# Kernel tuning notes

Measured on AMD Instinct MI355X. Metric: run time of the kernel, lower is better.

## Reference

```python
import jax, jax.numpy as jnp
import numpy as np

CHUNK = 2048  # i-tile size; each block kernel slab is CHUNK x M (128 MB fp32), never the full N x M


def setup_inputs() -> dict:
    key = jax.random.key(0)
    k1, k2, k3, k4 = jax.random.split(key, 4)
    ls = jax.random.uniform(k1, (1,), dtype=jnp.float32)          # scalar lengthscale g (Pm(0,1))
    x = jax.random.normal(k2, (16384, 32), dtype=jnp.float32)     # Vi points
    y = jax.random.normal(k3, (16384, 32), dtype=jnp.float32)     # Vj points
    b = jax.random.normal(k4, (16384, 16), dtype=jnp.float32)     # Vj RHS
    return {"ls": ls, "x": x, "y": y, "b": b}


def reference(ls, x, y, b):
    # out[i] = sum_j exp(-g * ||x_i - y_j||^2) * b[j]   (KeOps Genred Sum over axis=1)
    g = ls[0]
    N, D = x.shape
    yn = jnp.sum(y * y, axis=1)  # [M]

    def blk(xc):  # xc: [CHUNK, D]
        xn = jnp.sum(xc * xc, axis=1, keepdims=True)                   # [CHUNK, 1]
        sq = jnp.maximum(xn + yn[None, :] - 2.0 * (xc @ y.T), 0.0)     # [CHUNK, M]
        return jnp.exp(-g * sq) @ b                                    # [CHUNK, Dv]

    out = jax.lax.map(blk, x.reshape(N // CHUNK, CHUNK, D))
    return out.reshape(N, b.shape[1])
```

## Files before the change

### kernel.cpp

```cpp
#include <hip/hip_runtime.h>


#define NPTS 16384
#define D    32
#define DV   16
#define IBLK 256
#define JSPLIT 16
#define JBLK 64
#define NTILE  (NPTS / JBLK)
#define TILES  (NTILE / JSPLIT)
#define REC    12800
#define YH_OFF 256
#define YL_OFF 5376
#define BT_OFF 10496
#define PTS    72
#define PART_F4 (NPTS * DV / 4)

typedef _Float16 half8   __attribute__((ext_vector_type(8)));
typedef __fp16   cvt2_t  __attribute__((ext_vector_type(2)));
typedef float    float4_t __attribute__((ext_vector_type(4)));
typedef unsigned int u32;
typedef unsigned int u32x2 __attribute__((ext_vector_type(2)));

__device__ __forceinline__ void async16(const void* g, void* l) {
  __builtin_amdgcn_global_load_lds((const __attribute__((address_space(1))) u32*)g,
                                   (__attribute__((address_space(3))) u32*)l, 16, 0, 0);
}

__device__ __forceinline__ void stage_tile(const char* __restrict__ g,
                                           char* __restrict__ l, int tid) {
  async16(g + tid * 16,         l + tid * 16);
  async16(g + 4096 + tid * 16,  l + 4096 + tid * 16);
  async16(g + 8192 + tid * 16,  l + 8192 + tid * 16);
  if (tid < 32) async16(g + 12288 + tid * 16, l + 12288 + tid * 16);
}

__device__ __forceinline__ void permswap32(u32& a, u32& b) {
#if __has_builtin(__builtin_amdgcn_permlane32_swap)
  u32x2 r = __builtin_amdgcn_permlane32_swap(a, b, false, false);
  a = r[0]; b = r[1];
#else
  asm("v_permlane32_swap_b32 %0, %1" : "+v"(a), "+v"(b));
#endif
}

__device__ __forceinline__ void permswap16(u32& a, u32& b) {
#if __has_builtin(__builtin_amdgcn_permlane16_swap)
  u32x2 r = __builtin_amdgcn_permlane16_swap(a, b, false, false);
  a = r[0]; b = r[1];
#else
  asm("v_permlane16_swap_b32 %0, %1" : "+v"(a), "+v"(b));
#endif
}

__global__ __launch_bounds__(256) void rbf_prologue(
    const float* __restrict__ ls, const float* __restrict__ y,
    const float* __restrict__ b, char* __restrict__ rec0,
    float* __restrict__ outz, int zero_out) {
  __shared__ _Float16 sbt[256][17];
  const int tid = threadIdx.x;
  const int j = blockIdx.x * 256 + tid;
  const int tt = j >> 6, jloc = j & 63;
  char* rec = rec0 + (size_t)tt * REC;
  const float nl2g = -ls[0] * 1.4426950408889634f;

  const float4* yp = (const float4*)(y + (size_t)j * D);
  float s = 0.f;
  _Float16 hi[32], lo[32];
  #pragma unroll
  for (int c = 0; c < 8; ++c) {
    float4 v = yp[c];
    float f[4] = {v.x, v.y, v.z, v.w};
    #pragma unroll
    for (int k = 0; k < 4; ++k) {
      s = fmaf(f[k], f[k], s);
      _Float16 h = (_Float16)f[k];
      hi[c*4+k] = h;
      lo[c*4+k] = (_Float16)(f[k] - (float)h);
    }
  }
  ((float*)rec)[jloc] = nl2g * s;
  #pragma unroll
  for (int c = 0; c < 4; ++c) {
    *(half8*)(rec + YH_OFF + jloc * 80 + c * 16) = *(half8*)&hi[c*8];
    *(half8*)(rec + YL_OFF + jloc * 80 + c * 16) = *(half8*)&lo[c*8];
  }

  const float4* bp = (const float4*)(b + (size_t)j * DV);
  #pragma unroll
  for (int c = 0; c < 4; ++c) {
    float4 v = bp[c];
    sbt[tid][c*4+0] = (_Float16)v.x; sbt[tid][c*4+1] = (_Float16)v.y;
    sbt[tid][c*4+2] = (_Float16)v.z; sbt[tid][c*4+3] = (_Float16)v.w;
  }
  __syncthreads();
  #pragma unroll
  for (int r = 0; r < 2; ++r) {
    int cch = r * 256 + tid;
    int t4 = cch >> 7, rem = cch & 127, v = rem >> 3, jg = rem & 7;
    _Float16 tmp[8];
    #pragma unroll
    for (int k = 0; k < 8; ++k) tmp[k] = sbt[t4*64 + jg*8 + k][v];
    *(half8*)(rec0 + (size_t)(blockIdx.x*4 + t4)*REC + BT_OFF + v*144 + jg*16) =
        *(half8*)tmp;
  }

  if (zero_out) {
    float4 z = {0.f, 0.f, 0.f, 0.f};
    float4* ozp = (float4*)outz;
    #pragma unroll
    for (int r = 0; r < 4; ++r) ozp[blockIdx.x * 1024 + r * 256 + tid] = z;
  }
}

template <int MODE>
__global__ __launch_bounds__(256) void rbf_mfma(
    const float* __restrict__ ls, const float* __restrict__ x,
    const char* __restrict__ rec0, float* __restrict__ out,
    float* __restrict__ part) {
  __shared__ __align__(16) char SB[2][REC];

  const int tid  = threadIdx.x;
  const int lane = tid & 63, w = tid >> 6;
  const int t = lane & 15, q = lane >> 4;
  const int iblk = blockIdx.x & 63, jseg = blockIdx.x >> 6;
  const int tseg = jseg * TILES;

  const float nl2g = -ls[0] * 1.4426950408889634f;
  const float m2g  = -2.0f * nl2g;

  half8 xh[4], xl[4];
  float xns[4];
  #pragma unroll
  for (int f = 0; f < 4; ++f) {
    const int row = iblk * IBLK + f * 64 + w * 16 + t;
    const float4* xp = (const float4*)(x + (size_t)row * D + q * 8);
    float4 a0 = xp[0], a1 = xp[1];
    float fv[8] = {a0.x,a0.y,a0.z,a0.w,a1.x,a1.y,a1.z,a1.w};
    float s = 0.f;
    #pragma unroll
    for (int k = 0; k < 8; ++k) {
      s = fmaf(fv[k], fv[k], s);
      float vv = m2g * fv[k];
      _Float16 h = (_Float16)vv;
      xh[f][k] = h;
      xl[f][k] = (_Float16)(vv - (float)h);
    }
    s += __shfl_xor(s, 16);
    s += __shfl_xor(s, 32);
    xns[f] = fmaf(nl2g, s, 14.0f);
  }

  float4_t acc[4] = {{0,0,0,0},{0,0,0,0},{0,0,0,0},{0,0,0,0}};

  stage_tile(rec0 + (size_t)tseg * REC, &SB[0][0], tid);
  __syncthreads();

  for (int k = 0; k < TILES; ++k) {
    if (k + 1 < TILES)
      stage_tile(rec0 + (size_t)(tseg + k + 1) * REC, &SB[(k + 1) & 1][0], tid);

    const char* rec = &SB[k & 1][0];
    const float* ynp = (const float*)rec;
    const char* yhp = rec + YH_OFF;
    const char* ylp = rec + YL_OFF;
    const _Float16* btp = (const _Float16*)(rec + BT_OFF);

    half8 ah[4], al[4];
    float4_t yn4[4];
    #pragma unroll
    for (int s = 0; s < 4; ++s) {
      ah[s]  = *(const half8*)(yhp + (s * 16 + t) * 80 + q * 16);
      al[s]  = *(const half8*)(ylp + (s * 16 + t) * 80 + q * 16);
      yn4[s] = *(const float4_t*)(ynp + s * 16 + q * 4);
    }
    const half8 bh0 = *(const half8*)(btp + t * PTS + q * 8);
    const half8 bh1 = *(const half8*)(btp + t * PTS + 32 + q * 8);

    #pragma unroll
    for (int f = 0; f < 4; ++f) {
      u32 S[4][2];
      #pragma unroll
      for (int s = 0; s < 4; ++s) {
        float4_t e = {yn4[s][0] + xns[f], yn4[s][1] + xns[f],
                      yn4[s][2] + xns[f], yn4[s][3] + xns[f]};
        __builtin_amdgcn_s_setprio(1);
        e = __builtin_amdgcn_mfma_f32_16x16x32_f16(ah[s], xh[f], e, 0, 0, 0);
        e = __builtin_amdgcn_mfma_f32_16x16x32_f16(ah[s], xl[f], e, 0, 0, 0);
        e = __builtin_amdgcn_mfma_f32_16x16x32_f16(al[s], xh[f], e, 0, 0, 0);
        __builtin_amdgcn_s_setprio(0);
        float p0 = __builtin_amdgcn_exp2f(e[0]);
        float p1 = __builtin_amdgcn_exp2f(e[1]);
        float p2 = __builtin_amdgcn_exp2f(e[2]);
        float p3 = __builtin_amdgcn_exp2f(e[3]);
        union { cvt2_t c2; u32 u; } w0, w1;
        w0.c2 = __builtin_amdgcn_cvt_pkrtz(p0, p1);
        w1.c2 = __builtin_amdgcn_cvt_pkrtz(p2, p3);
        S[s][0] = w0.u; S[s][1] = w1.u;
      }
      u32 t0[4], t1[4];
      #pragma unroll
      for (int r = 0; r < 2; ++r) {
        u32 a = S[0][r], b = S[1][r];
        permswap32(a, b); permswap16(a, b);
        t0[r] = a; t0[2 + r] = b;
        a = S[2][r]; b = S[3][r];
        permswap32(a, b); permswap16(a, b);
        t1[r] = a; t1[2 + r] = b;
      }
      union { u32 u[4]; half8 h; } up0, up1;
      up0.u[0] = t0[0]; up0.u[1] = t0[1]; up0.u[2] = t0[2]; up0.u[3] = t0[3];
      up1.u[0] = t1[0]; up1.u[1] = t1[1]; up1.u[2] = t1[2]; up1.u[3] = t1[3];
      __builtin_amdgcn_s_setprio(1);
      acc[f] = __builtin_amdgcn_mfma_f32_16x16x32_f16(bh0, up0.h, acc[f], 0, 0, 0);
      acc[f] = __builtin_amdgcn_mfma_f32_16x16x32_f16(bh1, up1.h, acc[f], 0, 0, 0);
      __builtin_amdgcn_s_setprio(0);
    }
    __syncthreads();
  }

  const float sc = 0.00006103515625f;
  #pragma unroll
  for (int f = 0; f < 4; ++f) {
    const int row = iblk * IBLK + f * 64 + w * 16 + t;
    if (MODE == 0) {
      float* orow = out + (size_t)row * DV + q * 4;
      #pragma unroll
      for (int r = 0; r < 4; ++r) atomicAdd(&orow[r], acc[f][r] * sc);
    } else {
      float4_t st = acc[f] * sc;
      *(float4_t*)(part + ((size_t)jseg * NPTS + row) * DV + q * 4) = st;
    }
  }
}

__global__ __launch_bounds__(256) void rbf_reduce(
    const float4_t* __restrict__ part, float4_t* __restrict__ out) {
  const int i = blockIdx.x * 256 + threadIdx.x;
  float4_t s = part[i];
  #pragma unroll
  for (int k = 1; k < JSPLIT; ++k) s += part[(size_t)k * PART_F4 + i];
  out[i] = s;
}

#define BJ     128
#define BLOCK  256
#define FJSPLIT 32
#define SYP    36

__global__ __launch_bounds__(BLOCK) void rbf_fp32_kernel(
    const float* __restrict__ ls, const float* __restrict__ x,
    const float* __restrict__ y, const float* __restrict__ b,
    float* __restrict__ out, int N, int M) {
  __shared__ float sy[BJ * SYP];
  __shared__ float sb[BJ * DV];
  __shared__ float syn[BJ];
  const int itiles = N / BLOCK;
  const int itile  = blockIdx.x & (itiles - 1);
  const int jseg   = blockIdx.x / itiles;
  const int i      = itile * BLOCK + threadIdx.x;
  const int jlen   = M / FJSPLIT;
  const int j0     = jseg * jlen;
  const float g    = ls[0];
  const float nl2g = -g * 1.4426950408889634f;
  float xr[D]; float xn = 0.f;
  {
    const float4* xp = (const float4*)(x + (size_t)i * D);
    #pragma unroll
    for (int qq = 0; qq < D / 4; ++qq) {
      float4 v = xp[qq];
      xr[4*qq+0]=v.x; xr[4*qq+1]=v.y; xr[4*qq+2]=v.z; xr[4*qq+3]=v.w;
      xn += v.x*v.x + v.y*v.y + v.z*v.z + v.w*v.w;
    }
  }
  float acc[DV];
  #pragma unroll
  for (int v = 0; v < DV; ++v) acc[v] = 0.f;
  for (int jt = j0; jt < j0 + jlen; jt += BJ) {
    {
      const float4* src = (const float4*)(y + (size_t)jt * D);
      #pragma unroll
      for (int r = 0; r < (BJ * D / 4) / BLOCK; ++r) {
        int e4 = r * BLOCK + threadIdx.x;
        int j  = e4 >> 3; int dq = e4 & 7;
        *(float4*)&sy[j * SYP + dq * 4] = src[e4];
      }
      const float4* bsrc = (const float4*)(b + (size_t)jt * DV);
      #pragma unroll
      for (int r = 0; r < (BJ * DV / 4) / BLOCK; ++r) {
        int e4 = r * BLOCK + threadIdx.x;
        *(float4*)&sb[e4 * 4] = bsrc[e4];
      }
    }
    __syncthreads();
    if (threadIdx.x < BJ) {
      const float* row = &sy[threadIdx.x * SYP];
      float s0=0,s1=0,s2=0,s3=0;
      #pragma unroll
      for (int d = 0; d < D; d += 4) {
        s0=fmaf(row[d+0],row[d+0],s0); s1=fmaf(row[d+1],row[d+1],s1);
        s2=fmaf(row[d+2],row[d+2],s2); s3=fmaf(row[d+3],row[d+3],s3);
      }
      syn[threadIdx.x] = (s0+s1)+(s2+s3);
    }
    __syncthreads();
    #pragma unroll 2
    for (int j = 0; j < BJ; ++j) {
      const float* yrow = &sy[j * SYP];
      float d0=0,d1=0,d2=0,d3=0;
      #pragma unroll
      for (int d = 0; d < D; d += 4) {
        d0=fmaf(xr[d+0],yrow[d+0],d0); d1=fmaf(xr[d+1],yrow[d+1],d1);
        d2=fmaf(xr[d+2],yrow[d+2],d2); d3=fmaf(xr[d+3],yrow[d+3],d3);
      }
      float dot=(d0+d1)+(d2+d3);
      float sq = fmaxf(xn + syn[j] - 2.0f*dot, 0.0f);
      float p  = exp2f(nl2g * sq);
      const float* brow = &sb[j * DV];
      #pragma unroll
      for (int v = 0; v < DV; ++v) acc[v] = fmaf(p, brow[v], acc[v]);
    }
    __syncthreads();
  }
  float* orow = out + (size_t)i * DV;
  #pragma unroll
  for (int v = 0; v < DV; ++v) atomicAdd(&orow[v], acc[v]);
}

extern "C" void kernel_launch(void* const* d_in, const int* in_sizes, int n_in,
                              void* d_out, int out_size, void* d_ws, size_t ws_size,
                              hipStream_t stream) {
  const float* ls = (const float*)d_in[0];
  const float* x  = (const float*)d_in[1];
  const float* y  = (const float*)d_in[2];
  const float* b  = (const float*)d_in[3];
  float* out = (float*)d_out;

  const size_t need_rec  = (size_t)NTILE * REC;
  const size_t need_part = need_rec + (size_t)JSPLIT * NPTS * DV * 4;

  if (ws_size >= need_part) {
    char* rec0 = (char*)d_ws;
    float* part = (float*)(rec0 + need_rec);
    rbf_prologue<<<NPTS / 256, 256, 0, stream>>>(ls, y, b, rec0, out, 0);
    dim3 grid((NPTS / IBLK) * JSPLIT);
    rbf_mfma<1><<<grid, 256, 0, stream>>>(ls, x, rec0, out, part);
    rbf_reduce<<<PART_F4 / 256, 256, 0, stream>>>((const float4_t*)part,
                                                  (float4_t*)out);
  } else if (ws_size >= need_rec) {
    char* rec0 = (char*)d_ws;
    rbf_prologue<<<NPTS / 256, 256, 0, stream>>>(ls, y, b, rec0, out, 1);
    dim3 grid((NPTS / IBLK) * JSPLIT);
    rbf_mfma<0><<<grid, 256, 0, stream>>>(ls, x, rec0, out, nullptr);
  } else {
    (void)hipMemsetAsync(d_out, 0, (size_t)out_size * sizeof(float), stream);
    dim3 grid((NPTS / BLOCK) * FJSPLIT);
    rbf_fp32_kernel<<<grid, BLOCK, 0, stream>>>(ls, x, y, b, out, NPTS, NPTS);
  }
}
```

Baseline: 140.6 us.

## Fuse split-j reduction into MFMA kernel via last-block counter, use 32 j-splits

Removes the separate reduce kernel launch. Each i-block's partials are now summed by whichever j-split block finishes last, detected with a per-iblk atomic counter and threadfence. Counters are zeroed in the prologue. When workspace allows, the j-split is also raised from 16 to 32, giving 2048 blocks for better occupancy and tail balance. The cost is more partial traffic and serialized reduction work in the last blocks.

```diff
diff --git a/kernel.cpp b/kernel.cpp
--- a/kernel.cpp
+++ b/kernel.cpp
@@ -5,10 +5,8 @@
 #define D    32
 #define DV   16
 #define IBLK 256
-#define JSPLIT 16
 #define JBLK 64
 #define NTILE  (NPTS / JBLK)
-#define TILES  (NTILE / JSPLIT)
 #define REC    12800
 #define YH_OFF 256
 #define YL_OFF 5376
@@ -56,7 +54,7 @@
 __global__ __launch_bounds__(256) void rbf_prologue(
     const float* __restrict__ ls, const float* __restrict__ y,
     const float* __restrict__ b, char* __restrict__ rec0,
-    float* __restrict__ outz, int zero_out) {
+    float* __restrict__ outz, int zero_out, u32* __restrict__ cnt) {
   __shared__ _Float16 sbt[256][17];
   const int tid = threadIdx.x;
   const int j = blockIdx.x * 256 + tid;
@@ -64,6 +62,8 @@
   char* rec = rec0 + (size_t)tt * REC;
   const float nl2g = -ls[0] * 1.4426950408889634f;
 
+  if (cnt && tid == 0) cnt[blockIdx.x] = 0;
+
   const float4* yp = (const float4*)(y + (size_t)j * D);
   float s = 0.f;
   _Float16 hi[32], lo[32];
@@ -113,18 +113,20 @@
   }
 }
 
-template <int MODE>
+template <int JS, int MODE>
 __global__ __launch_bounds__(256) void rbf_mfma(
     const float* __restrict__ ls, const float* __restrict__ x,
     const char* __restrict__ rec0, float* __restrict__ out,
-    float* __restrict__ part) {
+    float* __restrict__ part, u32* __restrict__ cnt) {
+  constexpr int NT = NTILE / JS;
   __shared__ __align__(16) char SB[2][REC];
+  __shared__ int lastflag;
 
   const int tid  = threadIdx.x;
   const int lane = tid & 63, w = tid >> 6;
   const int t = lane & 15, q = lane >> 4;
   const int iblk = blockIdx.x & 63, jseg = blockIdx.x >> 6;
-  const int tseg = jseg * TILES;
+  const int tseg = jseg * NT;
 
   const float nl2g = -ls[0] * 1.4426950408889634f;
   const float m2g  = -2.0f * nl2g;
@@ -156,8 +158,8 @@
   stage_tile(rec0 + (size_t)tseg * REC, &SB[0][0], tid);
   __syncthreads();
 
-  for (int k = 0; k < TILES; ++k) {
-    if (k + 1 < TILES)
+  for (int k = 0; k < NT; ++k) {
+    if (k + 1 < NT)
       stage_tile(rec0 + (size_t)(tseg + k + 1) * REC, &SB[(k + 1) & 1][0], tid);
 
     const char* rec = &SB[k & 1][0];
@@ -220,27 +222,41 @@
   }
 
   const float sc = 0.00006103515625f;
-  #pragma unroll
-  for (int f = 0; f < 4; ++f) {
-    const int row = iblk * IBLK + f * 64 + w * 16 + t;
-    if (MODE == 0) {
+  if (MODE == 0) {
+    #pragma unroll
+    for (int f = 0; f < 4; ++f) {
+      const int row = iblk * IBLK + f * 64 + w * 16 + t;
       float* orow = out + (size_t)row * DV + q * 4;
       #pragma unroll
       for (int r = 0; r < 4; ++r) atomicAdd(&orow[r], acc[f][r] * sc);
-    } else {
+    }
+  } else {
+    #pragma unroll
+    for (int f = 0; f < 4; ++f) {
+      const int row = iblk * IBLK + f * 64 + w * 16 + t;
       float4_t st = acc[f] * sc;
       *(float4_t*)(part + ((size_t)jseg * NPTS + row) * DV + q * 4) = st;
     }
-  }
-}
-
-__global__ __launch_bounds__(256) void rbf_reduce(
-    const float4_t* __restrict__ part, float4_t* __restrict__ out) {
-  const int i = blockIdx.x * 256 + threadIdx.x;
-  float4_t s = part[i];
-  #pragma unroll
-  for (int k = 1; k < JSPLIT; ++k) s += part[(size_t)k * PART_F4 + i];
-  out[i] = s;
+    __threadfence();
+    if (tid == 0) {
+      u32 prev = atomicAdd(&cnt[iblk], 1u);
+      lastflag = (prev == (u32)(JS - 1));
+    }
+    __syncthreads();
+    if (lastflag) {
+      __threadfence();
+      const float4_t* pp = (const float4_t*)part;
+      float4_t* op = (float4_t*)out;
+      #pragma unroll
+      for (int r = 0; r < 4; ++r) {
+        const int idx = r * 256 + tid;
+        const size_t base = (size_t)iblk * 1024 + idx;
+        float4_t s = pp[base];
+        for (int k2 = 1; k2 < JS; ++k2) s += pp[(size_t)k2 * PART_F4 + base];
+        op[base] = s;
+      }
+    }
+  }
 }
 
 #define BJ     128
@@ -336,22 +352,27 @@
   const float* b  = (const float*)d_in[3];
   float* out = (float*)d_out;
 
-  const size_t need_rec  = (size_t)NTILE * REC;
-  const size_t need_part = need_rec + (size_t)JSPLIT * NPTS * DV * 4;
-
-  if (ws_size >= need_part) {
+  const size_t need_rec = (size_t)NTILE * REC;
+  const size_t slab     = (size_t)NPTS * DV * 4;
+  const size_t need32   = need_rec + 32 * slab + 256;
+  const size_t need16   = need_rec + 16 * slab + 256;
+
+  if (ws_size >= need32) {
     char* rec0 = (char*)d_ws;
     float* part = (float*)(rec0 + need_rec);
-    rbf_prologue<<<NPTS / 256, 256, 0, stream>>>(ls, y, b, rec0, out, 0);
-    dim3 grid((NPTS / IBLK) * JSPLIT);
-    rbf_mfma<1><<<grid, 256, 0, stream>>>(ls, x, rec0, out, part);
-    rbf_reduce<<<PART_F4 / 256, 256, 0, stream>>>((const float4_t*)part,
-                                                  (float4_t*)out);
+    u32* cnt = (u32*)(rec0 + need_rec + 32 * slab);
+    rbf_prologue<<<NPTS / 256, 256, 0, stream>>>(ls, y, b, rec0, out, 0, cnt);
+    rbf_mfma<32, 1><<<dim3(64 * 32), 256, 0, stream>>>(ls, x, rec0, out, part, cnt);
+  } else if (ws_size >= need16) {
+    char* rec0 = (char*)d_ws;
+    float* part = (float*)(rec0 + need_rec);
+    u32* cnt = (u32*)(rec0 + need_rec + 16 * slab);
+    rbf_prologue<<<NPTS / 256, 256, 0, stream>>>(ls, y, b, rec0, out, 0, cnt);
+    rbf_mfma<16, 1><<<dim3(64 * 16), 256, 0, stream>>>(ls, x, rec0, out, part, cnt);
   } else if (ws_size >= need_rec) {
     char* rec0 = (char*)d_ws;
-    rbf_prologue<<<NPTS / 256, 256, 0, stream>>>(ls, y, b, rec0, out, 1);
-    dim3 grid((NPTS / IBLK) * JSPLIT);
-    rbf_mfma<0><<<grid, 256, 0, stream>>>(ls, x, rec0, out, nullptr);
+    rbf_prologue<<<NPTS / 256, 256, 0, stream>>>(ls, y, b, rec0, out, 1, nullptr);
+    rbf_mfma<16, 0><<<dim3(64 * 16), 256, 0, stream>>>(ls, x, rec0, out, nullptr, nullptr);
   } else {
     (void)hipMemsetAsync(d_out, 0, (size_t)out_size * sizeof(float), stream);
     dim3 grid((NPTS / BLOCK) * FJSPLIT);
```

Result: slower. 396.8 us (+182.2%).
